# Optimization experiments

Measured on AMD Instinct MI355X. Metric: run time of the kernel, lower is better.

## Reference

```python
import jax, jax.numpy as jnp
import numpy as np

B, S, E, H = 2, 2048, 1024, 16
HD = E // H            # head_dim = 64
ROT = 64               # rotary_dim == head_dim
BASE = 10000.0


def setup_inputs() -> dict:
    key = jax.random.key(0)
    k1, k2, k3, k4, k5 = jax.random.split(key, 5)
    return {
        "x": jax.random.normal(k1, (B, S, E), dtype=jnp.float32),
        "mask": jnp.ones((B, S), dtype=jnp.int32),
        "qkv_w": jax.random.normal(k2, (3 * E, E), dtype=jnp.float32) * (1.0 / np.sqrt(E)),
        "qkv_b": jax.random.normal(k3, (3 * E,), dtype=jnp.float32) * 0.02,
        "out_w": jax.random.normal(k4, (E, E), dtype=jnp.float32) * (1.0 / np.sqrt(E)),
        "out_b": jax.random.normal(k5, (E,), dtype=jnp.float32) * 0.02,
    }


def _rotate_half(x):
    # split last dim into (even, odd) pairs and rotate 90 degrees
    x = x.reshape(*x.shape[:-1], -1, 2)
    x1, x2 = x[..., 0], x[..., 1]
    return jnp.stack((-x2, x1), axis=-1).reshape(*x.shape[:-2], -1)


def _rope_cos_sin(seq_len, rot_dim, dtype):
    inv_freq = 1.0 / (BASE ** (jnp.arange(0, rot_dim, 2, dtype=jnp.float32) / rot_dim))
    freqs = jnp.arange(seq_len, dtype=jnp.float32)[:, None] * inv_freq[None, :]  # [S, rot/2]
    cos = jnp.repeat(jnp.cos(freqs), 2, axis=-1).astype(dtype)  # [S, rot]
    sin = jnp.repeat(jnp.sin(freqs), 2, axis=-1).astype(dtype)
    return cos, sin


def reference(x, mask, qkv_w, qkv_b, out_w, out_b):
    b, s, _ = x.shape
    qkv = x @ qkv_w.T + qkv_b                      # [B,S,3E]
    q, k, v = jnp.split(qkv, 3, axis=-1)
    shape = lambda t: t.reshape(b, s, H, HD).transpose(0, 2, 1, 3)  # [B,H,S,HD]
    q, k, v = shape(q), shape(k), shape(v)

    cos, sin = _rope_cos_sin(s, ROT, q.dtype)      # [S, ROT]
    cos = cos[None, None]                          # [1,1,S,ROT]
    sin = sin[None, None]
    q_rot, q_pass = q[..., :ROT], q[..., ROT:]
    k_rot, k_pass = k[..., :ROT], k[..., ROT:]
    q = jnp.concatenate((q_rot * cos + _rotate_half(q_rot) * sin, q_pass), axis=-1)
    k = jnp.concatenate((k_rot * cos + _rotate_half(k_rot) * sin, k_pass), axis=-1)

    scale = 1.0 / np.sqrt(HD)
    scores = jnp.einsum("bhqd,bhkd->bhqk", q, k) * scale  # [B,H,S,S]
    keep = (mask != 0)[:, None, None, :]           # [B,1,1,S]
    scores = jnp.where(keep, scores, -jnp.inf)
    attn = jax.nn.softmax(scores, axis=-1)
    context = jnp.einsum("bhqk,bhkd->bhqd", attn, v)
    context = context.transpose(0, 2, 1, 3).reshape(b, s, E)
    return context @ out_w.T + out_b
```

## Files before the change

kernel.cpp:

```cpp
#include <hip/hip_runtime.h>
#include <hip/hip_bf16.h>
#include <cmath>

#define SB 2048
#define EB 1024
#define NH 16
#define HD 64
#define KLOG 0.14391156831212788f
#define QSC 0.18033688011112042f

typedef unsigned short u16;
typedef unsigned int u32;
typedef __attribute__((ext_vector_type(8))) short short8;
typedef __attribute__((ext_vector_type(4))) float f32x4;

__device__ __forceinline__ u16 f2b(float x) {
  __hip_bfloat16 h = __float2bfloat16(x);
  return *reinterpret_cast<u16*>(&h);
}

__device__ __forceinline__ u32 pkb(float lo, float hi) {
#if __has_builtin(__builtin_amdgcn_cvt_pk_bf16_f32)
  auto v = __builtin_amdgcn_cvt_pk_bf16_f32(lo, hi);
  u32 r;
  __builtin_memcpy(&r, &v, 4);
  return r;
#else
  return (u32)f2b(lo) | ((u32)f2b(hi) << 16);
#endif
}

__device__ __forceinline__ void gl_lds16(const u16* g, u16* l) {
  __builtin_amdgcn_global_load_lds(
      (const __attribute__((address_space(1))) unsigned int*)g,
      (__attribute__((address_space(3))) unsigned int*)l, 16, 0, 0);
}

#define CN1 (4096 * 1024 / 4)
#define CN2 (3072 * 1024 / 4)
#define CN3 (1024 * 1024 / 4)
#define CNS (CN1 + CN2 + CN3)
__global__ __launch_bounds__(256) void conv_all(
    const float* __restrict__ x, const float* __restrict__ w1,
    const float* __restrict__ w2, u16* __restrict__ xb,
    u16* __restrict__ wqb, u16* __restrict__ owb,
    float* __restrict__ ctab, float* __restrict__ stab) {
  int i = blockIdx.x * 256 + threadIdx.x;
  if (i < CNS) {
    const float* src;
    u16* dst;
    int j;
    if (i < CN1) { src = x; dst = xb; j = i; }
    else if (i < CN1 + CN2) { src = w1; dst = wqb; j = i - CN1; }
    else { src = w2; dst = owb; j = i - CN1 - CN2; }
    float4 v = ((const float4*)src)[j];
    ushort4 o;
    o.x = f2b(v.x); o.y = f2b(v.y); o.z = f2b(v.z); o.w = f2b(v.w);
    ((ushort4*)dst)[j] = o;
  } else {
    int j = i - CNS;
    if (j < SB * 32) {
      int pos = j >> 5, p = j & 31;
      float th = (float)pos * expf(-(float)(2 * p) * KLOG);
      float sn, cs;
      sincosf(th, &sn, &cs);
      ctab[j] = cs; stab[j] = sn;
    }
  }
}

__global__ __launch_bounds__(256) void qkv_mfma_rope(
    const u16* __restrict__ A, const u16* __restrict__ Bw,
    const float* __restrict__ bias, const float* __restrict__ ctab,
    const float* __restrict__ stab, u16* __restrict__ qb,
    u16* __restrict__ kb, u16* __restrict__ vt) {
  __shared__ u16 As[128 * 32];
  __shared__ u16 Bs[128 * 32];
  __shared__ float CS[128 * 32];
  __shared__ float SN[128 * 32];

  const int t = threadIdx.x;
  const int lane = t & 63, wv = t >> 6;
  const int l15 = lane & 15, quad = lane >> 4;
  const int wm = wv >> 1, wn = wv & 1;
  const int m0 = blockIdx.x * 128;
  const int n0 = blockIdx.y * 128;

  f32x4 acc[4][4] = {};

  for (int k0 = 0; k0 < 1024; k0 += 32) {
#pragma unroll
    for (int c = 0; c < 2; c++) {
      int r = wv * 32 + c * 16;
      const u16* ga = A + (size_t)(m0 + r + (lane >> 2)) * 1024 + k0 + (lane & 3) * 8;
      const u16* gb = Bw + (size_t)(n0 + r + (lane >> 2)) * 1024 + k0 + (lane & 3) * 8;
      gl_lds16(ga, &As[r * 32]);
      gl_lds16(gb, &Bs[r * 32]);
    }
    __syncthreads();

    short8 a[4], b[4];
#pragma unroll
    for (int mi = 0; mi < 4; mi++)
      a[mi] = *(const short8*)&As[(wm * 64 + mi * 16 + l15) * 32 + quad * 8];
#pragma unroll
    for (int ni = 0; ni < 4; ni++)
      b[ni] = *(const short8*)&Bs[(wn * 64 + ni * 16 + l15) * 32 + quad * 8];
#pragma unroll
    for (int mi = 0; mi < 4; mi++)
#pragma unroll
      for (int ni = 0; ni < 4; ni++)
        acc[mi][ni] = __builtin_amdgcn_mfma_f32_16x16x32_bf16(a[mi], b[ni], acc[mi][ni], 0, 0, 0);
    __syncthreads();
  }

  const int n_base = n0 + wn * 64;
  const int which = n_base >> 10;
  float b4[4];
#pragma unroll
  for (int ni = 0; ni < 4; ni++) b4[ni] = bias[n_base + ni * 16 + l15];

  {
    int base = (m0 & 2047) * 32;
#pragma unroll
    for (int i = 0; i < 4; i++) {
      int idx = (t + i * 256) * 4;
      *(float4*)&CS[idx] = *(const float4*)&ctab[base + idx];
      *(float4*)&SN[idx] = *(const float4*)&stab[base + idx];
    }
  }
  __syncthreads();

  const int h = (n_base & 1023) >> 6;
  const int bb = m0 >> 11;
  if (which < 2) {
    u16* dst = (which == 0) ? qb : kb;
#pragma unroll
    for (int mi = 0; mi < 4; mi++) {
#pragma unroll
      for (int r = 0; r < 4; r++) {
        int row = wm * 64 + mi * 16 + quad * 4 + r;
        int s = (m0 & 2047) + row;
        size_t obase = ((size_t)(bb * NH + h) * SB + s) * HD;
#pragma unroll
        for (int ni = 0; ni < 4; ni++) {
          float v = acc[mi][ni][r] + b4[ni];
          int d = ni * 16 + l15;
          float pv = __shfl_xor(v, 1, 64);
          float c = CS[row * 32 + (d >> 1)];
          float sn_ = SN[row * 32 + (d >> 1)];
          v = v * c + pv * ((d & 1) ? sn_ : -sn_);
          if (which == 0) v *= QSC;
          dst[obase + d] = f2b(v);
        }
      }
    }
  } else {
    size_t tbase = (size_t)(bb * NH + h) * HD;
#pragma unroll
    for (int mi = 0; mi < 4; mi++) {
      int s0 = (m0 & 2047) + wm * 64 + mi * 16 + quad * 4;
#pragma unroll
      for (int ni = 0; ni < 4; ni++) {
        int d = ni * 16 + l15;
        u32 p0 = pkb(acc[mi][ni][0] + b4[ni], acc[mi][ni][1] + b4[ni]);
        u32 p1 = pkb(acc[mi][ni][2] + b4[ni], acc[mi][ni][3] + b4[ni]);
        uint2 pk = make_uint2(p0, p1);
        *(uint2*)&vt[(tbase + d) * SB + s0] = pk;
      }
    }
  }
}

__global__ __launch_bounds__(512, 4) void attn_mfma(
    const u16* __restrict__ qb, const u16* __restrict__ kb,
    const u16* __restrict__ vt, const int* __restrict__ mask,
    u16* __restrict__ ctx) {
  __shared__ u16 Ks[2][64][72];
  __shared__ u16 Vt[2][64][72];
  __shared__ u32 Ps2[8][32][20];
  __shared__ float fbs[2][64];

  const int bh = blockIdx.x, b = bh >> 4, h = bh & 15;
  const int q0 = blockIdx.y * 128;
  const int t = threadIdx.x;
  const int lane = t & 63, wv = t >> 6;
  const int l15 = lane & 15, quad = lane >> 4;

  short8 bq[2];
  {
    const u16* qp = qb + ((size_t)bh * SB + q0 + wv * 16 + l15) * HD;
    bq[0] = *(const short8*)&qp[quad * 8];
    bq[1] = *(const short8*)&qp[32 + quad * 8];
  }

  const u16* kbase = kb + (size_t)bh * SB * HD;
  const u16* vbase = vt + (size_t)bh * HD * SB;
  const int* mbase = mask + b * SB;

  const int sr = t >> 3, sc = t & 7;

  uint4 kreg = *(const uint4*)&kbase[(size_t)sr * HD + sc * 8];
  uint4 vreg = *(const uint4*)&vbase[(size_t)sr * SB + sc * 8];
  float freg = (t < 64) ? (mbase[t] ? 0.f : -1e9f) : 0.f;

  f32x4 o[4] = {};
  float l_i = 0.f;

  for (int kt = 0; kt < SB / 64; kt++) {
    const int bufi = kt & 1;
    *(uint4*)&Ks[bufi][sr][sc * 8] = kreg;
    *(uint4*)&Vt[bufi][sr][sc * 8] = vreg;
    if (t < 64) fbs[bufi][t] = freg;
    __syncthreads();

    if (kt + 1 < SB / 64) {
      kreg = *(const uint4*)&kbase[(size_t)((kt + 1) * 64 + sr) * HD + sc * 8];
      vreg = *(const uint4*)&vbase[(size_t)sr * SB + (kt + 1) * 64 + sc * 8];
      if (t < 64) freg = mbase[(kt + 1) * 64 + t] ? 0.f : -1e9f;
    }

    f32x4 s[4];
#pragma unroll
    for (int mb = 0; mb < 4; mb++) {
      short8 a0 = *(const short8*)&Ks[bufi][mb * 16 + l15][quad * 8];
      short8 a1 = *(const short8*)&Ks[bufi][mb * 16 + l15][32 + quad * 8];
      f32x4 z = {};
      z = __builtin_amdgcn_mfma_f32_16x16x32_bf16(a0, bq[0], z, 0, 0, 0);
      s[mb] = __builtin_amdgcn_mfma_f32_16x16x32_bf16(a1, bq[1], s[mb] = z, 0, 0, 0);
    }

#pragma unroll
    for (int mb = 0; mb < 4; mb++) {
      f32x4 bias4 = *(const f32x4*)&fbs[bufi][mb * 16 + quad * 4];
#pragma unroll
      for (int r = 0; r < 4; r++) {
        float p = __builtin_amdgcn_exp2f(s[mb][r] + bias4[r]);
        s[mb][r] = p;
        l_i += p;
      }
    }

#pragma unroll
    for (int mb = 0; mb < 4; mb++)
#pragma unroll
      for (int pr = 0; pr < 2; pr++)
        Ps2[wv][mb * 8 + quad * 2 + pr][l15] = pkb(s[mb][2 * pr], s[mb][2 * pr + 1]);
    short8 pb[2];
#pragma unroll
    for (int kk = 0; kk < 2; kk++) {
      u32 w[4];
#pragma unroll
      for (int j = 0; j < 4; j++)
        w[j] = Ps2[wv][kk * 16 + quad * 4 + j][l15];
      pb[kk] = *(const short8*)w;
    }

#pragma unroll
    for (int nb = 0; nb < 4; nb++) {
      short8 v0 = *(const short8*)&Vt[bufi][nb * 16 + l15][quad * 8];
      short8 v1 = *(const short8*)&Vt[bufi][nb * 16 + l15][32 + quad * 8];
      o[nb] = __builtin_amdgcn_mfma_f32_16x16x32_bf16(v0, pb[0], o[nb], 0, 0, 0);
      o[nb] = __builtin_amdgcn_mfma_f32_16x16x32_bf16(v1, pb[1], o[nb], 0, 0, 0);
    }
  }

  l_i += __shfl_xor(l_i, 16, 64);
  l_i += __shfl_xor(l_i, 32, 64);

  {
    float linv = 1.f / l_i;
    int qrow = q0 + wv * 16 + l15;
    size_t base = ((size_t)b * SB + qrow) * EB + h * HD;
#pragma unroll
    for (int nb = 0; nb < 4; nb++)
#pragma unroll
      for (int pr = 0; pr < 2; pr++) {
        int d = nb * 16 + quad * 4 + 2 * pr;
        *(u32*)&ctx[base + d] =
            pkb(o[nb][2 * pr] * linv, o[nb][2 * pr + 1] * linv);
      }
  }
}

__global__ __launch_bounds__(256) void out_mfma(
    const u16* __restrict__ A, const u16* __restrict__ Bw,
    const float* __restrict__ bias, float* __restrict__ out) {
  __shared__ u16 As[64 * 32];
  __shared__ u16 Bs[128 * 32];

  const int t = threadIdx.x;
  const int lane = t & 63, wv = t >> 6;
  const int l15 = lane & 15, quad = lane >> 4;
  const int wm = wv >> 1, wn = wv & 1;
  const int m0 = blockIdx.x * 64;
  const int n0 = blockIdx.y * 128;

  f32x4 acc[2][4] = {};

  for (int k0 = 0; k0 < 1024; k0 += 32) {
    {
      const u16* ga = A + (size_t)(m0 + wv * 16 + (lane >> 2)) * 1024 + k0 + (lane & 3) * 8;
      gl_lds16(ga, &As[(wv * 16) * 32]);
#pragma unroll
      for (int c = 0; c < 2; c++) {
        int r = wv * 32 + c * 16;
        const u16* gb = Bw + (size_t)(n0 + r + (lane >> 2)) * 1024 + k0 + (lane & 3) * 8;
        gl_lds16(gb, &Bs[r * 32]);
      }
    }
    __syncthreads();

    short8 a[2], b[4];
#pragma unroll
    for (int mi = 0; mi < 2; mi++)
      a[mi] = *(const short8*)&As[(wm * 32 + mi * 16 + l15) * 32 + quad * 8];
#pragma unroll
    for (int ni = 0; ni < 4; ni++)
      b[ni] = *(const short8*)&Bs[(wn * 64 + ni * 16 + l15) * 32 + quad * 8];
#pragma unroll
    for (int mi = 0; mi < 2; mi++)
#pragma unroll
      for (int ni = 0; ni < 4; ni++)
        acc[mi][ni] = __builtin_amdgcn_mfma_f32_16x16x32_bf16(a[mi], b[ni], acc[mi][ni], 0, 0, 0);
    __syncthreads();
  }

  float b4[4];
#pragma unroll
  for (int ni = 0; ni < 4; ni++) b4[ni] = bias[n0 + wn * 64 + ni * 16 + l15];
#pragma unroll
  for (int mi = 0; mi < 2; mi++)
#pragma unroll
    for (int r = 0; r < 4; r++) {
      int m = m0 + wm * 32 + mi * 16 + quad * 4 + r;
#pragma unroll
      for (int ni = 0; ni < 4; ni++)
        out[(size_t)m * 1024 + n0 + wn * 64 + ni * 16 + l15] = acc[mi][ni][r] + b4[ni];
    }
}

extern "C" void kernel_launch(void* const* d_in, const int* in_sizes, int n_in,
                              void* d_out, int out_size, void* d_ws, size_t ws_size,
                              hipStream_t stream) {
  const float* x     = (const float*)d_in[0];
  const int* mask    = (const int*)d_in[1];
  const float* qkv_w = (const float*)d_in[2];
  const float* qkv_b = (const float*)d_in[3];
  const float* out_w = (const float*)d_in[4];
  const float* out_b = (const float*)d_in[5];
  float* out = (float*)d_out;

  char* wsb = (char*)d_ws;
  u16* xb    = (u16*)wsb;
  u16* wqb   = (u16*)(wsb + ( 8ull << 20));
  u16* owb   = (u16*)(wsb + (14ull << 20));
  u16* qb    = (u16*)(wsb + (16ull << 20));
  u16* kb    = (u16*)(wsb + (24ull << 20));
  u16* vtb   = (u16*)(wsb + (32ull << 20));
  u16* cxb   = (u16*)(wsb + (40ull << 20));
  float* ctab = (float*)(wsb + (48ull << 20));
  float* stab = (float*)(wsb + (48ull << 20) + (256u << 10));

  dim3 blk(256);
  int convBlocks = (CNS + SB * 32 + 255) / 256;
  hipLaunchKernelGGL(conv_all, dim3(convBlocks), blk, 0, stream,
                     x, qkv_w, out_w, xb, wqb, owb, ctab, stab);

  hipLaunchKernelGGL(qkv_mfma_rope, dim3(32, 24), blk, 0, stream,
                     xb, wqb, qkv_b, ctab, stab, qb, kb, vtb);

  hipLaunchKernelGGL(attn_mfma, dim3(32, 16), dim3(512), 0, stream,
                     qb, kb, vtb, mask, cxb);

  hipLaunchKernelGGL(out_mfma, dim3(64, 8), blk, 0, stream, cxb, owb, out_b, out);
}
```

Measured before the change: 213.4 us.

## Give attention waves two query tiles each and stage V-transpose stores through LDS

The attention kernel now runs 256 threads per block, and each wave handles 32 query rows (two 16-row tiles) instead of 16. Each K/V fragment read from LDS is therefore reused for twice as many MFMAs, and the block count stays the same. The P-matrix shuffle through LDS now uses a row-major layout with vector stores and loads. In the QKV kernel, V-output blocks skip the rope table load and transpose their tile through shared memory, so the global writes to vt become coalesced 16-byte rows. The cost is more registers per thread and fewer waves per block to hide latency.

```diff
diff --git a/kernel.cpp b/kernel.cpp
--- a/kernel.cpp
+++ b/kernel.cpp
@@ -74,10 +74,12 @@
     const float* __restrict__ bias, const float* __restrict__ ctab,
     const float* __restrict__ stab, u16* __restrict__ qb,
     u16* __restrict__ kb, u16* __restrict__ vt) {
-  __shared__ u16 As[128 * 32];
-  __shared__ u16 Bs[128 * 32];
-  __shared__ float CS[128 * 32];
-  __shared__ float SN[128 * 32];
+  __shared__ char smem[49152];
+  u16* As   = (u16*)smem;
+  u16* Bs   = (u16*)(smem + 8192);
+  float* CS = (float*)(smem + 16384);
+  float* SN = (float*)(smem + 32768);
+  u32* T32  = (u32*)smem;
 
   const int t = threadIdx.x;
   const int lane = t & 63, wv = t >> 6;
@@ -115,25 +117,25 @@
   }
 
   const int n_base = n0 + wn * 64;
-  const int which = n_base >> 10;
+  const int which = n0 >> 10;
   float b4[4];
 #pragma unroll
   for (int ni = 0; ni < 4; ni++) b4[ni] = bias[n_base + ni * 16 + l15];
-
-  {
-    int base = (m0 & 2047) * 32;
-#pragma unroll
-    for (int i = 0; i < 4; i++) {
-      int idx = (t + i * 256) * 4;
-      *(float4*)&CS[idx] = *(const float4*)&ctab[base + idx];
-      *(float4*)&SN[idx] = *(const float4*)&stab[base + idx];
-    }
-  }
-  __syncthreads();
 
   const int h = (n_base & 1023) >> 6;
   const int bb = m0 >> 11;
+
   if (which < 2) {
+    {
+      int base = (m0 & 2047) * 32;
+#pragma unroll
+      for (int i = 0; i < 4; i++) {
+        int idx = (t + i * 256) * 4;
+        *(float4*)&CS[idx] = *(const float4*)&ctab[base + idx];
+        *(float4*)&SN[idx] = *(const float4*)&stab[base + idx];
+      }
+    }
+    __syncthreads();
     u16* dst = (which == 0) ? qb : kb;
 #pragma unroll
     for (int mi = 0; mi < 4; mi++) {
@@ -156,29 +158,34 @@
       }
     }
   } else {
-    size_t tbase = (size_t)(bb * NH + h) * HD;
-#pragma unroll
-    for (int mi = 0; mi < 4; mi++) {
-      int s0 = (m0 & 2047) + wm * 64 + mi * 16 + quad * 4;
+#pragma unroll
+    for (int mi = 0; mi < 4; mi++)
 #pragma unroll
       for (int ni = 0; ni < 4; ni++) {
-        int d = ni * 16 + l15;
-        u32 p0 = pkb(acc[mi][ni][0] + b4[ni], acc[mi][ni][1] + b4[ni]);
-        u32 p1 = pkb(acc[mi][ni][2] + b4[ni], acc[mi][ni][3] + b4[ni]);
-        uint2 pk = make_uint2(p0, p1);
-        *(uint2*)&vt[(tbase + d) * SB + s0] = pk;
-      }
-    }
-  }
-}
-
-__global__ __launch_bounds__(512, 4) void attn_mfma(
+        int n = wn * 64 + ni * 16 + l15;
+        int inner = wm * 32 + mi * 8 + quad * 2;
+        T32[n * 68 + inner]     = pkb(acc[mi][ni][0] + b4[ni], acc[mi][ni][1] + b4[ni]);
+        T32[n * 68 + inner + 1] = pkb(acc[mi][ni][2] + b4[ni], acc[mi][ni][3] + b4[ni]);
+      }
+    __syncthreads();
+    const u16* T = (const u16*)smem;
+    int n = t >> 1;
+    int c = n0 + n - 2048;
+    int hh = c >> 6, d = c & 63;
+    size_t rowb = ((size_t)(bb * NH + hh) * HD + d) * SB + (m0 & 2047) + (t & 1) * 64;
+#pragma unroll
+    for (int j = 0; j < 8; j++)
+      *(uint4*)&vt[rowb + j * 8] = *(const uint4*)&T[n * 136 + (t & 1) * 64 + j * 8];
+  }
+}
+
+__global__ __launch_bounds__(256, 4) void attn_mfma(
     const u16* __restrict__ qb, const u16* __restrict__ kb,
     const u16* __restrict__ vt, const int* __restrict__ mask,
     u16* __restrict__ ctx) {
   __shared__ u16 Ks[2][64][72];
   __shared__ u16 Vt[2][64][72];
-  __shared__ u32 Ps2[8][32][20];
+  __shared__ u32 Ps2[4][16][34];
   __shared__ float fbs[2][64];
 
   const int bh = blockIdx.x, b = bh >> 4, h = bh & 15;
@@ -187,47 +194,63 @@
   const int lane = t & 63, wv = t >> 6;
   const int l15 = lane & 15, quad = lane >> 4;
 
-  short8 bq[2];
-  {
-    const u16* qp = qb + ((size_t)bh * SB + q0 + wv * 16 + l15) * HD;
-    bq[0] = *(const short8*)&qp[quad * 8];
-    bq[1] = *(const short8*)&qp[32 + quad * 8];
+  short8 bq[2][2];
+#pragma unroll
+  for (int qh = 0; qh < 2; qh++) {
+    const u16* qp = qb + ((size_t)bh * SB + q0 + wv * 32 + qh * 16 + l15) * HD;
+    bq[qh][0] = *(const short8*)&qp[quad * 8];
+    bq[qh][1] = *(const short8*)&qp[32 + quad * 8];
   }
 
   const u16* kbase = kb + (size_t)bh * SB * HD;
   const u16* vbase = vt + (size_t)bh * HD * SB;
   const int* mbase = mask + b * SB;
 
-  const int sr = t >> 3, sc = t & 7;
-
-  uint4 kreg = *(const uint4*)&kbase[(size_t)sr * HD + sc * 8];
-  uint4 vreg = *(const uint4*)&vbase[(size_t)sr * SB + sc * 8];
-  float freg = (t < 64) ? (mbase[t] ? 0.f : -1e9f) : 0.f;
-
-  f32x4 o[4] = {};
-  float l_i = 0.f;
+  uint4 kreg[2], vreg[2];
+  float freg;
+#pragma unroll
+  for (int i = 0; i < 2; i++) {
+    int c = t + 256 * i;
+    kreg[i] = *(const uint4*)&kbase[(size_t)(c >> 3) * HD + (c & 7) * 8];
+    vreg[i] = *(const uint4*)&vbase[(size_t)(c >> 3) * SB + (c & 7) * 8];
+  }
+  freg = (t < 64) ? (mbase[t] ? 0.f : -1e9f) : 0.f;
+
+  f32x4 o[2][4] = {};
+  float l_i[2] = {0.f, 0.f};
 
   for (int kt = 0; kt < SB / 64; kt++) {
     const int bufi = kt & 1;
-    *(uint4*)&Ks[bufi][sr][sc * 8] = kreg;
-    *(uint4*)&Vt[bufi][sr][sc * 8] = vreg;
+#pragma unroll
+    for (int i = 0; i < 2; i++) {
+      int c = t + 256 * i;
+      *(uint4*)&Ks[bufi][c >> 3][(c & 7) * 8] = kreg[i];
+      *(uint4*)&Vt[bufi][c >> 3][(c & 7) * 8] = vreg[i];
+    }
     if (t < 64) fbs[bufi][t] = freg;
     __syncthreads();
 
     if (kt + 1 < SB / 64) {
-      kreg = *(const uint4*)&kbase[(size_t)((kt + 1) * 64 + sr) * HD + sc * 8];
-      vreg = *(const uint4*)&vbase[(size_t)sr * SB + (kt + 1) * 64 + sc * 8];
-      if (t < 64) freg = mbase[(kt + 1) * 64 + t] ? 0.f : -1e9f;
-    }
-
-    f32x4 s[4];
+      size_t ko = (size_t)(kt + 1) * 64;
+#pragma unroll
+      for (int i = 0; i < 2; i++) {
+        int c = t + 256 * i;
+        kreg[i] = *(const uint4*)&kbase[(ko + (c >> 3)) * HD + (c & 7) * 8];
+        vreg[i] = *(const uint4*)&vbase[(size_t)(c >> 3) * SB + ko + (c & 7) * 8];
+      }
+      freg = (t < 64) ? (mbase[ko + t] ? 0.f : -1e9f) : 0.f;
+    }
+
+    f32x4 s0[4], s1[4];
 #pragma unroll
     for (int mb = 0; mb < 4; mb++) {
       short8 a0 = *(const short8*)&Ks[bufi][mb * 16 + l15][quad * 8];
       short8 a1 = *(const short8*)&Ks[bufi][mb * 16 + l15][32 + quad * 8];
-      f32x4 z = {};
-      z = __builtin_amdgcn_mfma_f32_16x16x32_bf16(a0, bq[0], z, 0, 0, 0);
-      s[mb] = __builtin_amdgcn_mfma_f32_16x16x32_bf16(a1, bq[1], s[mb] = z, 0, 0, 0);
+      f32x4 z0 = {}, z1 = {};
+      z0 = __builtin_amdgcn_mfma_f32_16x16x32_bf16(a0, bq[0][0], z0, 0, 0, 0);
+      s0[mb] = __builtin_amdgcn_mfma_f32_16x16x32_bf16(a1, bq[0][1], z0, 0, 0, 0);
+      z1 = __builtin_amdgcn_mfma_f32_16x16x32_bf16(a0, bq[1][0], z1, 0, 0, 0);
+      s1[mb] = __builtin_amdgcn_mfma_f32_16x16x32_bf16(a1, bq[1][1], z1, 0, 0, 0);
     }
 
 #pragma unroll
@@ -235,42 +258,49 @@
       f32x4 bias4 = *(const f32x4*)&fbs[bufi][mb * 16 + quad * 4];
 #pragma unroll
       for (int r = 0; r < 4; r++) {
-        float p = __builtin_amdgcn_exp2f(s[mb][r] + bias4[r]);
-        s[mb][r] = p;
-        l_i += p;
-      }
-    }
-
-#pragma unroll
-    for (int mb = 0; mb < 4; mb++)
-#pragma unroll
-      for (int pr = 0; pr < 2; pr++)
-        Ps2[wv][mb * 8 + quad * 2 + pr][l15] = pkb(s[mb][2 * pr], s[mb][2 * pr + 1]);
-    short8 pb[2];
-#pragma unroll
-    for (int kk = 0; kk < 2; kk++) {
-      u32 w[4];
-#pragma unroll
-      for (int j = 0; j < 4; j++)
-        w[j] = Ps2[wv][kk * 16 + quad * 4 + j][l15];
-      pb[kk] = *(const short8*)w;
-    }
+        float p0 = __builtin_amdgcn_exp2f(s0[mb][r] + bias4[r]);
+        float p1 = __builtin_amdgcn_exp2f(s1[mb][r] + bias4[r]);
+        s0[mb][r] = p0; l_i[0] += p0;
+        s1[mb][r] = p1; l_i[1] += p1;
+      }
+    }
+
+    short8 pb0[2], pb1[2];
+#pragma unroll
+    for (int mb = 0; mb < 4; mb++) {
+      uint2 w2 = make_uint2(pkb(s0[mb][0], s0[mb][1]), pkb(s0[mb][2], s0[mb][3]));
+      *(uint2*)&Ps2[wv][l15][8 * mb + 2 * quad] = w2;
+    }
+#pragma unroll
+    for (int kk = 0; kk < 2; kk++)
+      pb0[kk] = *(const short8*)&Ps2[wv][l15][kk * 16 + 4 * quad];
+#pragma unroll
+    for (int mb = 0; mb < 4; mb++) {
+      uint2 w2 = make_uint2(pkb(s1[mb][0], s1[mb][1]), pkb(s1[mb][2], s1[mb][3]));
+      *(uint2*)&Ps2[wv][l15][8 * mb + 2 * quad] = w2;
+    }
+#pragma unroll
+    for (int kk = 0; kk < 2; kk++)
+      pb1[kk] = *(const short8*)&Ps2[wv][l15][kk * 16 + 4 * quad];
 
 #pragma unroll
     for (int nb = 0; nb < 4; nb++) {
       short8 v0 = *(const short8*)&Vt[bufi][nb * 16 + l15][quad * 8];
       short8 v1 = *(const short8*)&Vt[bufi][nb * 16 + l15][32 + quad * 8];
-      o[nb] = __builtin_amdgcn_mfma_f32_16x16x32_bf16(v0, pb[0], o[nb], 0, 0, 0);
-      o[nb] = __builtin_amdgcn_mfma_f32_16x16x32_bf16(v1, pb[1], o[nb], 0, 0, 0);
-    }
-  }
-
-  l_i += __shfl_xor(l_i, 16, 64);
-  l_i += __shfl_xor(l_i, 32, 64);
-
-  {
-    float linv = 1.f / l_i;
-    int qrow = q0 + wv * 16 + l15;
+      o[0][nb] = __builtin_amdgcn_mfma_f32_16x16x32_bf16(v0, pb0[0], o[0][nb], 0, 0, 0);
+      o[0][nb] = __builtin_amdgcn_mfma_f32_16x16x32_bf16(v1, pb0[1], o[0][nb], 0, 0, 0);
+      o[1][nb] = __builtin_amdgcn_mfma_f32_16x16x32_bf16(v0, pb1[0], o[1][nb], 0, 0, 0);
+      o[1][nb] = __builtin_amdgcn_mfma_f32_16x16x32_bf16(v1, pb1[1], o[1][nb], 0, 0, 0);
+    }
+  }
+
+#pragma unroll
+  for (int qh = 0; qh < 2; qh++) {
+    float l = l_i[qh];
+    l += __shfl_xor(l, 16, 64);
+    l += __shfl_xor(l, 32, 64);
+    float linv = 1.f / l;
+    int qrow = q0 + wv * 32 + qh * 16 + l15;
     size_t base = ((size_t)b * SB + qrow) * EB + h * HD;
 #pragma unroll
     for (int nb = 0; nb < 4; nb++)
@@ -278,7 +308,7 @@
       for (int pr = 0; pr < 2; pr++) {
         int d = nb * 16 + quad * 4 + 2 * pr;
         *(u32*)&ctx[base + d] =
-            pkb(o[nb][2 * pr] * linv, o[nb][2 * pr + 1] * linv);
+            pkb(o[qh][nb][2 * pr] * linv, o[qh][nb][2 * pr + 1] * linv);
       }
   }
 }
@@ -370,7 +400,7 @@
   hipLaunchKernelGGL(qkv_mfma_rope, dim3(32, 24), blk, 0, stream,
                      xb, wqb, qkv_b, ctab, stab, qb, kb, vtb);
 
-  hipLaunchKernelGGL(attn_mfma, dim3(32, 16), dim3(512), 0, stream,
+  hipLaunchKernelGGL(attn_mfma, dim3(32, 16), blk, 0, stream,
                      qb, kb, vtb, mask, cxb);
 
   hipLaunchKernelGGL(out_mfma, dim3(64, 8), blk, 0, stream, cxb, owb, out_b, out);
```

Result: slower. 237.8 us (+11.4%).

## Stream K/V tiles directly into swizzled LDS and precompute mask bias

Applied to the files above, without the earlier changes.

The attention kernel now fills its K and V tiles with asynchronous global-to-LDS loads into an XOR-swizzled, unpadded layout, replacing the register staging and the explicit LDS stores. The mask bias is precomputed once in the conversion kernel and read straight from global memory instead of being staged through shared memory. The P-matrix LDS transpose is restructured to use wider vector writes and reads. The intent is to cut VGPR pressure, LDS store instructions and bank conflicts in the inner loop. In exchange, correctness depends on the async load completing before the single barrier, and the global bias reads add memory traffic.

```diff
diff --git a/kernel.cpp b/kernel.cpp
--- a/kernel.cpp
+++ b/kernel.cpp
@@ -42,9 +42,10 @@
 #define CNS (CN1 + CN2 + CN3)
 __global__ __launch_bounds__(256) void conv_all(
     const float* __restrict__ x, const float* __restrict__ w1,
-    const float* __restrict__ w2, u16* __restrict__ xb,
-    u16* __restrict__ wqb, u16* __restrict__ owb,
-    float* __restrict__ ctab, float* __restrict__ stab) {
+    const float* __restrict__ w2, const int* __restrict__ mask,
+    u16* __restrict__ xb, u16* __restrict__ wqb, u16* __restrict__ owb,
+    float* __restrict__ ctab, float* __restrict__ stab,
+    float* __restrict__ fbias) {
   int i = blockIdx.x * 256 + threadIdx.x;
   if (i < CNS) {
     const float* src;
@@ -65,6 +66,9 @@
       float sn, cs;
       sincosf(th, &sn, &cs);
       ctab[j] = cs; stab[j] = sn;
+    } else {
+      int j2 = j - SB * 32;
+      if (j2 < 2 * SB) fbias[j2] = mask[j2] ? 0.f : -1e9f;
     }
   }
 }
@@ -174,12 +178,11 @@
 
 __global__ __launch_bounds__(512, 4) void attn_mfma(
     const u16* __restrict__ qb, const u16* __restrict__ kb,
-    const u16* __restrict__ vt, const int* __restrict__ mask,
+    const u16* __restrict__ vt, const float* __restrict__ fbias,
     u16* __restrict__ ctx) {
-  __shared__ u16 Ks[2][64][72];
-  __shared__ u16 Vt[2][64][72];
-  __shared__ u32 Ps2[8][32][20];
-  __shared__ float fbs[2][64];
+  __shared__ u16 Ks[2][4096];
+  __shared__ u16 Vt[2][4096];
+  __shared__ u32 Ps2[8][16][34];
 
   const int bh = blockIdx.x, b = bh >> 4, h = bh & 15;
   const int q0 = blockIdx.y * 128;
@@ -196,43 +199,42 @@
 
   const u16* kbase = kb + (size_t)bh * SB * HD;
   const u16* vbase = vt + (size_t)bh * HD * SB;
-  const int* mbase = mask + b * SB;
-
-  const int sr = t >> 3, sc = t & 7;
-
-  uint4 kreg = *(const uint4*)&kbase[(size_t)sr * HD + sc * 8];
-  uint4 vreg = *(const uint4*)&vbase[(size_t)sr * SB + sc * 8];
-  float freg = (t < 64) ? (mbase[t] ? 0.f : -1e9f) : 0.f;
+  const float* fbase = fbias + b * SB;
+
+  const int srow = lane >> 3;
+  const int schunk = ((lane & 7) ^ srow) * 8;
+  const int fslot = quad ^ (l15 & 7);
+
+  gl_lds16(kbase + (size_t)(wv * 8 + srow) * HD + schunk, &Ks[0][wv * 512]);
+  gl_lds16(vbase + (size_t)(wv * 8 + srow) * SB + schunk, &Vt[0][wv * 512]);
 
   f32x4 o[4] = {};
   float l_i = 0.f;
 
   for (int kt = 0; kt < SB / 64; kt++) {
     const int bufi = kt & 1;
-    *(uint4*)&Ks[bufi][sr][sc * 8] = kreg;
-    *(uint4*)&Vt[bufi][sr][sc * 8] = vreg;
-    if (t < 64) fbs[bufi][t] = freg;
     __syncthreads();
 
     if (kt + 1 < SB / 64) {
-      kreg = *(const uint4*)&kbase[(size_t)((kt + 1) * 64 + sr) * HD + sc * 8];
-      vreg = *(const uint4*)&vbase[(size_t)sr * SB + (kt + 1) * 64 + sc * 8];
-      if (t < 64) freg = mbase[(kt + 1) * 64 + t] ? 0.f : -1e9f;
+      size_t ko = (size_t)(kt + 1) * 64;
+      gl_lds16(kbase + (ko + wv * 8 + srow) * HD + schunk, &Ks[1 - bufi][wv * 512]);
+      gl_lds16(vbase + (size_t)(wv * 8 + srow) * SB + ko + schunk, &Vt[1 - bufi][wv * 512]);
     }
 
     f32x4 s[4];
 #pragma unroll
     for (int mb = 0; mb < 4; mb++) {
-      short8 a0 = *(const short8*)&Ks[bufi][mb * 16 + l15][quad * 8];
-      short8 a1 = *(const short8*)&Ks[bufi][mb * 16 + l15][32 + quad * 8];
+      const u16* kr = &Ks[bufi][(mb * 16 + l15) * 64];
+      short8 a0 = *(const short8*)&kr[fslot * 8];
+      short8 a1 = *(const short8*)&kr[(fslot ^ 4) * 8];
       f32x4 z = {};
       z = __builtin_amdgcn_mfma_f32_16x16x32_bf16(a0, bq[0], z, 0, 0, 0);
-      s[mb] = __builtin_amdgcn_mfma_f32_16x16x32_bf16(a1, bq[1], s[mb] = z, 0, 0, 0);
+      s[mb] = __builtin_amdgcn_mfma_f32_16x16x32_bf16(a1, bq[1], z, 0, 0, 0);
     }
 
 #pragma unroll
     for (int mb = 0; mb < 4; mb++) {
-      f32x4 bias4 = *(const f32x4*)&fbs[bufi][mb * 16 + quad * 4];
+      f32x4 bias4 = *(const f32x4*)&fbase[kt * 64 + mb * 16 + quad * 4];
 #pragma unroll
       for (int r = 0; r < 4; r++) {
         float p = __builtin_amdgcn_exp2f(s[mb][r] + bias4[r]);
@@ -242,24 +244,20 @@
     }
 
 #pragma unroll
-    for (int mb = 0; mb < 4; mb++)
-#pragma unroll
-      for (int pr = 0; pr < 2; pr++)
-        Ps2[wv][mb * 8 + quad * 2 + pr][l15] = pkb(s[mb][2 * pr], s[mb][2 * pr + 1]);
+    for (int mb = 0; mb < 4; mb++) {
+      uint2 w2 = make_uint2(pkb(s[mb][0], s[mb][1]), pkb(s[mb][2], s[mb][3]));
+      *(uint2*)&Ps2[wv][l15][8 * mb + 2 * quad] = w2;
+    }
     short8 pb[2];
 #pragma unroll
-    for (int kk = 0; kk < 2; kk++) {
-      u32 w[4];
-#pragma unroll
-      for (int j = 0; j < 4; j++)
-        w[j] = Ps2[wv][kk * 16 + quad * 4 + j][l15];
-      pb[kk] = *(const short8*)w;
-    }
+    for (int kk = 0; kk < 2; kk++)
+      pb[kk] = *(const short8*)&Ps2[wv][l15][kk * 16 + 4 * quad];
 
 #pragma unroll
     for (int nb = 0; nb < 4; nb++) {
-      short8 v0 = *(const short8*)&Vt[bufi][nb * 16 + l15][quad * 8];
-      short8 v1 = *(const short8*)&Vt[bufi][nb * 16 + l15][32 + quad * 8];
+      const u16* vr = &Vt[bufi][(nb * 16 + l15) * 64];
+      short8 v0 = *(const short8*)&vr[fslot * 8];
+      short8 v1 = *(const short8*)&vr[(fslot ^ 4) * 8];
       o[nb] = __builtin_amdgcn_mfma_f32_16x16x32_bf16(v0, pb[0], o[nb], 0, 0, 0);
       o[nb] = __builtin_amdgcn_mfma_f32_16x16x32_bf16(v1, pb[1], o[nb], 0, 0, 0);
     }
@@ -361,17 +359,18 @@
   u16* cxb   = (u16*)(wsb + (40ull << 20));
   float* ctab = (float*)(wsb + (48ull << 20));
   float* stab = (float*)(wsb + (48ull << 20) + (256u << 10));
+  float* fbias = (float*)(wsb + (48ull << 20) + (512u << 10));
 
   dim3 blk(256);
-  int convBlocks = (CNS + SB * 32 + 255) / 256;
+  int convBlocks = (CNS + SB * 32 + 2 * SB + 255) / 256;
   hipLaunchKernelGGL(conv_all, dim3(convBlocks), blk, 0, stream,
-                     x, qkv_w, out_w, xb, wqb, owb, ctab, stab);
+                     x, qkv_w, out_w, mask, xb, wqb, owb, ctab, stab, fbias);
 
   hipLaunchKernelGGL(qkv_mfma_rope, dim3(32, 24), blk, 0, stream,
                      xb, wqb, qkv_b, ctab, stab, qb, kb, vtb);
 
   hipLaunchKernelGGL(attn_mfma, dim3(32, 16), dim3(512), 0, stream,
-                     qb, kb, vtb, mask, cxb);
+                     qb, kb, vtb, fbias, cxb);
 
   hipLaunchKernelGGL(out_mfma, dim3(64, 8), blk, 0, stream, cxb, owb, out_b, out);
 }
```

Result: no change. 212.4 us (-0.5%).
